# Optimization experiments

Measured on AMD Instinct MI355X. Metric: run time of the kernel, lower is better.

Reference implementation:

```python
import jax, jax.numpy as jnp
import numpy as np

B, T, C, U = 16, 128, 64, 128
ODE_UNFOLDS = 6
EPS = 1e-8


def setup_inputs() -> dict:
    key = jax.random.key(0)
    ks = jax.random.split(key, 12)
    u = lambda k, s, lo, hi: jax.random.uniform(k, s, jnp.float32, lo, hi)
    return dict(
        x=jax.random.normal(ks[0], (B, T, C), jnp.float32),
        h0=jnp.zeros((B, U), jnp.float32),
        gleak=u(ks[1], (U,), 0.001, 1.0),
        vleak=u(ks[2], (U,), -0.2, 0.2),
        cm=u(ks[3], (U,), 0.4, 0.6),
        sigma=u(ks[4], (U, U), 3.0, 8.0),
        mu=u(ks[5], (U, U), 0.3, 0.8),
        w=u(ks[6], (U, U), 0.001, 1.0),
        erev=jnp.sign(jax.random.normal(ks[7], (U, U))).astype(jnp.float32),
        sensory_sigma=u(ks[8], (C, U), 3.0, 8.0),
        sensory_mu=u(ks[9], (C, U), 0.3, 0.8),
        sensory_w=u(ks[10], (C, U), 0.001, 1.0),
        sensory_erev=jnp.sign(jax.random.normal(ks[11], (C, U))).astype(jnp.float32),
        input_w=jnp.ones((C,), jnp.float32),
        input_b=jnp.zeros((C,), jnp.float32),
        output_w=jnp.ones((U,), jnp.float32),
        output_b=jnp.zeros((U,), jnp.float32),
    )


def reference(x, h0, gleak, vleak, cm, sigma, mu, w, erev,
              sensory_sigma, sensory_mu, sensory_w, sensory_erev,
              input_w, input_b, output_w, output_b):
    sp = jax.nn.softplus
    # Positive-constrained params (implicit_param_constraints=True)
    w_pos = sp(w)                      # [U,U]
    sw_pos = sp(sensory_w)             # [C,U]
    gl = sp(gleak)                     # [U]
    # elapsed_time ts = 1.0 -> cm_t = softplus(cm) / (1/ode_unfolds)
    cm_t = sp(cm) * ODE_UNFOLDS        # [U]

    def step(h, xt):
        # input affine mapping
        xt = xt * input_w + input_b                                        # [B,C]
        # sensory synapses (constant across unfolds)
        sens_act = sw_pos * jax.nn.sigmoid(sensory_sigma * (xt[:, :, None] - sensory_mu))  # [B,C,U]
        w_num_s = jnp.sum(sens_act * sensory_erev, axis=1)                 # [B,U]
        w_den_s = jnp.sum(sens_act, axis=1)                                # [B,U]
        v = h
        for _ in range(ODE_UNFOLDS):
            # recurrent synapses: pre dim 1, post dim 2
            w_act = w_pos * jax.nn.sigmoid(sigma * (v[:, :, None] - mu))   # [B,U,U]
            w_num = jnp.sum(w_act * erev, axis=1) + w_num_s                # [B,U]
            w_den = jnp.sum(w_act, axis=1) + w_den_s                       # [B,U]
            num = cm_t * v + gl * vleak + w_num
            den = cm_t + gl + w_den
            v = num / (den + EPS)
        out = v * output_w + output_b   # motor_size == units for FullyConnected
        return v, out

    h_final, outs = jax.lax.scan(step, h0, jnp.swapaxes(x, 0, 1))  # outs: [T,B,U]
    readout = jnp.swapaxes(outs, 0, 1)                             # [B,T,U]
    return readout, h_final
```

## Files before the change

kernel.cpp:

```cpp
#include <hip/hip_runtime.h>

#define NB 16
#define NT 128
#define NC 64
#define NU 128
#define UNFOLDS 6
#define LTC_EPS 1e-8f
#define LOG2E 1.44269504088896340736f
#define LN2   0.69314718055994530942f

typedef float f32x2 __attribute__((ext_vector_type(2)));

__device__ __forceinline__ float fast_softplus(float x) {
    return LN2 * __builtin_amdgcn_logf(1.0f + __builtin_amdgcn_exp2f(x * LOG2E));
}

template<int CTRL>
__device__ __forceinline__ float qperm(float x) {
    return __int_as_float(__builtin_amdgcn_update_dpp(
        0, __float_as_int(x), CTRL, 0xF, 0xF, true));
}
__device__ __forceinline__ float sum8(float x) {
    x += qperm<0xB1>(x);
    x += qperm<0x4E>(x);
    x += qperm<0x141>(x);
    return x;
}

__global__ __launch_bounds__(128)
void ltc_sens_kernel(const float* __restrict__ x,
                     const float* __restrict__ ssigma,
                     const float* __restrict__ smu,
                     const float* __restrict__ sw,
                     const float* __restrict__ serev,
                     const float* __restrict__ iw,
                     const float* __restrict__ ib,
                     float2* __restrict__ sens)
{
    __shared__ float xt[NC];
    const int blk = blockIdx.x;
    const int b = blk >> 7;
    const int t = blk & (NT - 1);
    const int j = threadIdx.x;
    if (j < NC) xt[j] = fmaf(x[(b * NT + t) * NC + j], iw[j], ib[j]);
    __syncthreads();

    float n0 = 0.f, n1 = 0.f, d0 = 0.f, d1 = 0.f;
#pragma unroll 8
    for (int c = 0; c < NC; ++c) {
        const int idx = c * NU + j;
        float sg = ssigma[idx];
        float m  = smu[idx];
        float wp = fast_softplus(sw[idx]);
        float er = serev[idx];
        float tt = (m - xt[c]) * (sg * LOG2E);
        float e  = __builtin_amdgcn_exp2f(tt);
        float r  = __builtin_amdgcn_rcpf(1.0f + e);
        float wr = wp * r;
        if (c & 1) { n1 = fmaf(wr, er, n1); d1 += wr; }
        else       { n0 = fmaf(wr, er, n0); d0 += wr; }
    }
    sens[(b * NT + t) * NU + j] = make_float2(n0 + n1, d0 + d1);
}

__global__ __launch_bounds__(1024, 4)
void ltc_seq_kernel(const float* __restrict__ h0,
                    const float* __restrict__ gleak,
                    const float* __restrict__ vleak,
                    const float* __restrict__ cm,
                    const float* __restrict__ sigma,
                    const float* __restrict__ mu,
                    const float* __restrict__ w,
                    const float* __restrict__ erev,
                    const float* __restrict__ ow,
                    const float* __restrict__ ob,
                    const float2* __restrict__ sens,
                    float* __restrict__ out)
{
    __shared__ __align__(16) float v_lds[2][NU];

    const int tid = threadIdx.x;
    const int b   = blockIdx.x;
    const int j   = tid >> 3;
    const int k   = tid & 7;

    f32x2 rA2[8], rB2[8], rW2[8], aW2[8];
#pragma unroll
    for (int m = 0; m < 4; ++m) {
        const int rot = (m + k) & 3;
#pragma unroll
        for (int h = 0; h < 2; ++h) {
            const int c   = 2 * m + h;
            const int i0  = (k << 4) + (rot << 2) + 2 * h;
            const int id0 = i0 * NU + j;
            const int id1 = id0 + NU;
            const float sg0 = sigma[id0], sg1 = sigma[id1];
            const float m0  = mu[id0],    m1  = mu[id1];
            const float wp0 = fast_softplus(w[id0]), wp1 = fast_softplus(w[id1]);
            const float er0 = erev[id0],  er1 = erev[id1];
            f32x2 a;  a.x = -sg0 * LOG2E;  a.y = -sg1 * LOG2E;
            f32x2 bb; bb.x = -a.x * m0;    bb.y = -a.y * m1;
            f32x2 ww; ww.x = wp0 * er0;    ww.y = wp1 * er1;
            f32x2 aw; aw.x = wp0;          aw.y = wp1;
            rA2[c] = a; rB2[c] = bb; rW2[c] = ww; aW2[c] = aw;
        }
    }

    const float cmt    = 6.0f * fast_softplus(cm[j]);
    const float gl     = fast_softplus(gleak[j]);
    const float glv    = gl * vleak[j];
    const float cmt_gl = cmt + gl + LTC_EPS;
    const float owj    = ow[j];
    const float obj    = ob[j];
    float vj = h0[b * NU + j];
    if (k == 0) v_lds[0][j] = vj;
    __syncthreads();

    int p = 0;
    float2 s_cur = sens[b * NT * NU + j];

    for (int t = 0; t < NT; ++t) {
#pragma unroll
        for (int q = 0; q < 8; ++q) {
            asm volatile("" : "+v"(rA2[q]), "+v"(rB2[q]), "+v"(rW2[q]), "+v"(aW2[q]));
        }

        const float nb = 0.125f * (s_cur.x + glv);
        const float db = 0.125f * (s_cur.y + cmt_gl);
        const int tn = (t + 1 < NT) ? (t + 1) : t;
        const float2 s_next = sens[(b * NT + tn) * NU + j];

#pragma unroll
        for (int u = 0; u < UNFOLDS; ++u) {
            f32x2 n2 = {nb, 0.f};
            f32x2 d2 = {db, 0.f};
#pragma unroll
            for (int m = 0; m < 4; ++m) {
                const float4 vv = *(const float4*)&v_lds[p][(k << 4) + (((m + k) & 3) << 2)];
                const f32x2 v0 = {vv.x, vv.y};
                const f32x2 v1 = {vv.z, vv.w};
                const f32x2 t0 = rA2[2 * m] * v0 + rB2[2 * m];
                const f32x2 t1 = rA2[2 * m + 1] * v1 + rB2[2 * m + 1];
                f32x2 e0, e1;
                e0.x = __builtin_amdgcn_exp2f(t0.x);
                e0.y = __builtin_amdgcn_exp2f(t0.y);
                e1.x = __builtin_amdgcn_exp2f(t1.x);
                e1.y = __builtin_amdgcn_exp2f(t1.y);
                const f32x2 one = {1.0f, 1.0f};
                const f32x2 u0 = e0 + one;
                const f32x2 u1 = e1 + one;
                const float p01 = u0.x * u0.y;
                const float p23 = u1.x * u1.y;
                const float rall = __builtin_amdgcn_rcpf(p01 * p23);
                const float r01 = rall * p23;
                const float r23 = rall * p01;
                const f32x2 rr0 = {r01, r01};
                const f32x2 rr1 = {r23, r23};
                const f32x2 r0 = rr0 * __builtin_shufflevector(u0, u0, 1, 0);
                const f32x2 r1 = rr1 * __builtin_shufflevector(u1, u1, 1, 0);
                n2 = rW2[2 * m] * r0 + n2;
                n2 = rW2[2 * m + 1] * r1 + n2;
                d2 = aW2[2 * m] * r0 + d2;
                d2 = aW2[2 * m + 1] * r1 + d2;
            }
            const float wn = sum8(n2.x + n2.y);
            const float wd = sum8(d2.x + d2.y);
            const float numf = fmaf(cmt, vj, wn);
            vj = numf * __builtin_amdgcn_rcpf(wd);
            if (k == 0) v_lds[p ^ 1][j] = vj;
            __syncthreads();
            p ^= 1;
        }

        if (k == 0) out[(b * NT + t) * NU + j] = fmaf(vj, owj, obj);
        s_cur = s_next;
    }
    if (k == 0) out[NB * NT * NU + b * NU + j] = vj;
}

extern "C" void kernel_launch(void* const* d_in, const int* in_sizes, int n_in,
                              void* d_out, int out_size, void* d_ws, size_t ws_size,
                              hipStream_t stream) {
    const float* x      = (const float*)d_in[0];
    const float* h0     = (const float*)d_in[1];
    const float* gleak  = (const float*)d_in[2];
    const float* vleak  = (const float*)d_in[3];
    const float* cm     = (const float*)d_in[4];
    const float* sigma  = (const float*)d_in[5];
    const float* mu     = (const float*)d_in[6];
    const float* w      = (const float*)d_in[7];
    const float* erev   = (const float*)d_in[8];
    const float* ssig   = (const float*)d_in[9];
    const float* smu    = (const float*)d_in[10];
    const float* sw     = (const float*)d_in[11];
    const float* serev  = (const float*)d_in[12];
    const float* iw     = (const float*)d_in[13];
    const float* ibv    = (const float*)d_in[14];
    const float* ow     = (const float*)d_in[15];
    const float* ob     = (const float*)d_in[16];
    float* out = (float*)d_out;

    float2* sens = (float2*)d_ws;
    ltc_sens_kernel<<<NB * NT, 128, 0, stream>>>(x, ssig, smu, sw, serev, iw, ibv, sens);
    ltc_seq_kernel<<<NB, 1024, 0, stream>>>(h0, gleak, vleak, cm, sigma, mu, w, erev,
                                            ow, ob, (const float2*)sens, out);
}
```

Baseline: 783.3 us.

## Replace hardware exp2 with packed polynomial exp2 and restructure sigmoid batching

Replaces the transcendental exp2 instructions in the recurrent inner loop with a degree-4 polynomial exp2 using rint, packed FMAs and ldexp. This moves work from the transcendental unit to the packed FMA pipe. It also regroups the reciprocal sharing into pairs of four-element products, splits the accumulators in two to shorten dependency chains, and changes the LDS rotation pattern to key on k>>1. The polynomial lowers exp2 accuracy and adds instruction count, and the reciprocal pairing risks overflow when the product of four (1+e) terms gets large.

```diff
diff --git a/kernel.cpp b/kernel.cpp
--- a/kernel.cpp
+++ b/kernel.cpp
@@ -87,7 +87,7 @@
     f32x2 rA2[8], rB2[8], rW2[8], aW2[8];
 #pragma unroll
     for (int m = 0; m < 4; ++m) {
-        const int rot = (m + k) & 3;
+        const int rot = (m + (k >> 1)) & 3;
 #pragma unroll
         for (int h = 0; h < 2; ++h) {
             const int c   = 2 * m + h;
@@ -132,37 +132,82 @@
 
 #pragma unroll
         for (int u = 0; u < UNFOLDS; ++u) {
-            f32x2 n2 = {nb, 0.f};
-            f32x2 d2 = {db, 0.f};
-#pragma unroll
-            for (int m = 0; m < 4; ++m) {
-                const float4 vv = *(const float4*)&v_lds[p][(k << 4) + (((m + k) & 3) << 2)];
-                const f32x2 v0 = {vv.x, vv.y};
-                const f32x2 v1 = {vv.z, vv.w};
-                const f32x2 t0 = rA2[2 * m] * v0 + rB2[2 * m];
-                const f32x2 t1 = rA2[2 * m + 1] * v1 + rB2[2 * m + 1];
-                f32x2 e0, e1;
-                e0.x = __builtin_amdgcn_exp2f(t0.x);
-                e0.y = __builtin_amdgcn_exp2f(t0.y);
-                e1.x = __builtin_amdgcn_exp2f(t1.x);
-                e1.y = __builtin_amdgcn_exp2f(t1.y);
+            f32x2 n2a = {nb, 0.f}, n2b = {0.f, 0.f};
+            f32x2 d2a = {db, 0.f}, d2b = {0.f, 0.f};
+#pragma unroll
+            for (int h4 = 0; h4 < 2; ++h4) {
+                const int mA = 2 * h4, mB = 2 * h4 + 1;
+                const int rotA = (mA + (k >> 1)) & 3;
+                const int rotB = (mB + (k >> 1)) & 3;
+                const float4 vvA = *(const float4*)&v_lds[p][(k << 4) + (rotA << 2)];
+                const float4 vvB = *(const float4*)&v_lds[p][(k << 4) + (rotB << 2)];
+                const f32x2 vA0 = {vvA.x, vvA.y};
+                const f32x2 vA1 = {vvA.z, vvA.w};
+                const f32x2 vB0 = {vvB.x, vvB.y};
+                const f32x2 vB1 = {vvB.z, vvB.w};
+                const f32x2 tA0 = rA2[2 * mA] * vA0 + rB2[2 * mA];
+                const f32x2 tA1 = rA2[2 * mA + 1] * vA1 + rB2[2 * mA + 1];
+                const f32x2 tB0 = rA2[2 * mB] * vB0 + rB2[2 * mB];
+                const f32x2 tB1 = rA2[2 * mB + 1] * vB1 + rB2[2 * mB + 1];
+
+#define SOFT_EXP2(tt, ee)                                                   \
+                {                                                           \
+                    const float nn0 = __builtin_rintf((tt).x);              \
+                    const float nn1 = __builtin_rintf((tt).y);              \
+                    f32x2 nf; nf.x = nn0; nf.y = nn1;                       \
+                    const f32x2 ff = (tt) - nf;                             \
+                    const f32x2 c4v = {0.009618129f, 0.009618129f};         \
+                    const f32x2 c3v = {0.055504109f, 0.055504109f};         \
+                    const f32x2 c2v = {0.240226507f, 0.240226507f};         \
+                    const f32x2 c1v = {0.693147181f, 0.693147181f};         \
+                    const f32x2 c0v = {1.0f, 1.0f};                         \
+                    f32x2 gg = c4v * ff + c3v;                              \
+                    gg = gg * ff + c2v;                                     \
+                    gg = gg * ff + c1v;                                     \
+                    gg = gg * ff + c0v;                                     \
+                    (ee).x = __builtin_amdgcn_ldexpf(gg.x, (int)nn0);       \
+                    (ee).y = __builtin_amdgcn_ldexpf(gg.y, (int)nn1);       \
+                }
+                f32x2 eA0, eA1, eB0, eB1;
+                SOFT_EXP2(tA0, eA0)
+                SOFT_EXP2(tA1, eA1)
+                SOFT_EXP2(tB0, eB0)
+                SOFT_EXP2(tB1, eB1)
+#undef SOFT_EXP2
+
                 const f32x2 one = {1.0f, 1.0f};
-                const f32x2 u0 = e0 + one;
-                const f32x2 u1 = e1 + one;
-                const float p01 = u0.x * u0.y;
-                const float p23 = u1.x * u1.y;
-                const float rall = __builtin_amdgcn_rcpf(p01 * p23);
-                const float r01 = rall * p23;
-                const float r23 = rall * p01;
-                const f32x2 rr0 = {r01, r01};
-                const f32x2 rr1 = {r23, r23};
-                const f32x2 r0 = rr0 * __builtin_shufflevector(u0, u0, 1, 0);
-                const f32x2 r1 = rr1 * __builtin_shufflevector(u1, u1, 1, 0);
-                n2 = rW2[2 * m] * r0 + n2;
-                n2 = rW2[2 * m + 1] * r1 + n2;
-                d2 = aW2[2 * m] * r0 + d2;
-                d2 = aW2[2 * m + 1] * r1 + d2;
+                const f32x2 uA0 = eA0 + one;
+                const f32x2 uA1 = eA1 + one;
+                const f32x2 uB0 = eB0 + one;
+                const f32x2 uB1 = eB1 + one;
+
+                {
+                    const f32x2 p2 = uA0 * uA1;
+                    const float P  = p2.x * p2.y;
+                    const float R  = __builtin_amdgcn_rcpf(P);
+                    f32x2 rr; rr.x = R * p2.y; rr.y = R * p2.x;
+                    const f32x2 r0 = rr * uA1;
+                    const f32x2 r1 = rr * uA0;
+                    n2a = rW2[2 * mA] * r0 + n2a;
+                    n2b = rW2[2 * mA + 1] * r1 + n2b;
+                    d2a = aW2[2 * mA] * r0 + d2a;
+                    d2b = aW2[2 * mA + 1] * r1 + d2b;
+                }
+                {
+                    const f32x2 p2 = uB0 * uB1;
+                    const float P  = p2.x * p2.y;
+                    const float R  = __builtin_amdgcn_rcpf(P);
+                    f32x2 rr; rr.x = R * p2.y; rr.y = R * p2.x;
+                    const f32x2 r0 = rr * uB1;
+                    const f32x2 r1 = rr * uB0;
+                    n2a = rW2[2 * mB] * r0 + n2a;
+                    n2b = rW2[2 * mB + 1] * r1 + n2b;
+                    d2a = aW2[2 * mB] * r0 + d2a;
+                    d2b = aW2[2 * mB + 1] * r1 + d2b;
+                }
             }
+            const f32x2 n2 = n2a + n2b;
+            const f32x2 d2 = d2a + d2b;
             const float wn = sum8(n2.x + n2.y);
             const float wd = sum8(d2.x + d2.y);
             const float numf = fmaf(cmt, vj, wn);
```

New measurement: 986.2 us. +25.9%, slower.
